# Kernel optimization log

Measured on AMD Instinct MI355X. Metric: run time of the kernel, lower is better.

## Reference

```python
import jax, jax.numpy as jnp
import numpy as np

N, E = 50000, 600000
DIN, DMID, DATTR, DOUT, DEMB, DH, K = 128, 128, 32, 128, 256, 768, 16


def setup_inputs() -> dict:
    key = jax.random.key(0)
    ks = jax.random.split(key, 12)
    s = lambda d: 1.0 / np.sqrt(d)
    return {
        "x": jax.random.normal(ks[0], (N, DIN), jnp.float32),
        "attributes": jax.random.normal(ks[1], (N, DATTR), jnp.float32),
        "edge_weight": jax.random.uniform(ks[2], (E,), jnp.float32),
        "hidden_state": jax.random.normal(ks[3], (1, DH), jnp.float32),
        "edge_index": jax.random.randint(ks[4], (2, E), 0, N, jnp.int64),
        "W1": jax.random.normal(ks[5], (DIN, DMID), jnp.float32) * s(DIN),
        "b1": jnp.zeros((DMID,), jnp.float32),
        "W2": jax.random.normal(ks[6], (DMID + DATTR, DOUT), jnp.float32) * s(DMID + DATTR),
        "b2": jnp.zeros((DOUT,), jnp.float32),
        "Wmap": jax.random.normal(ks[7], (DOUT + DATTR, DEMB), jnp.float32) * s(DOUT + DATTR),
        "bmap": jnp.zeros((DEMB,), jnp.float32),
        "Wattn": jax.random.normal(ks[8], (DH, DOUT + DATTR), jnp.float32) * s(DH),
    }


def gcn_conv(x, W, b, src, dst, w, n):
    """PyG GCNConv with normalize=True: A_hat = D^-1/2 (A+I) D^-1/2, out = A_hat X W + b."""
    loop = jnp.arange(n, dtype=src.dtype)
    src2 = jnp.concatenate([src, loop])
    dst2 = jnp.concatenate([dst, loop])
    w2 = jnp.concatenate([w, jnp.ones((n,), x.dtype)])
    deg = jax.ops.segment_sum(w2, dst2, num_segments=n)
    dinv = jnp.where(deg > 0, jax.lax.rsqrt(jnp.maximum(deg, 1e-12)), 0.0)
    norm = dinv[src2] * w2 * dinv[dst2]        # [E+N]
    h = x @ W                                   # [n, out] transform first (small dim)
    msg = h[src2] * norm[:, None]               # gather + scale, [E+N, out]
    return jax.ops.segment_sum(msg, dst2, num_segments=n) + b


def reference(x, attributes, edge_weight, hidden_state, edge_index,
              W1, b1, W2, b2, Wmap, bmap, Wattn):
    n = x.shape[0]
    src, dst = edge_index[0], edge_index[1]
    h = jax.nn.relu(gcn_conv(x, W1, b1, src, dst, edge_weight, n))
    # F.dropout with training=False is identity (module run in eval mode)
    h = jnp.concatenate([h, attributes], axis=1)           # [N, DMID+DATTR]
    h = gcn_conv(h, W2, b2, src, dst, edge_weight, n)      # [N, DOUT]
    h = jnp.concatenate([h, attributes], axis=1)           # [N, DOUT+DATTR]
    # DotAttnChoseImportentNode: project hidden state, dot with node feats, take top-K nodes
    q = hidden_state @ Wattn                                # [1, DOUT+DATTR]
    scores = h @ q[0]                                       # [N]
    _, idx = jax.lax.top_k(scores, K)
    chose_nodes = h[idx].reshape(1, -1)                     # [1, K*(DOUT+DATTR)]
    # final_mapping: mean-pool graph embed + linear
    emb = jnp.mean(h, axis=0, keepdims=True) @ Wmap + bmap  # [1, DEMB]
    return jnp.concatenate([emb, chose_nodes], axis=1)      # [1, DEMB + K*(DOUT+DATTR)]
```

## Files before the change

### kernel.cpp

```cpp
#include <hip/hip_runtime.h>

#define N_NODES 50000
#define N_EDGES 600000
#define D_IN 128
#define D_MID 128
#define D_ATTR 32
#define D_OUT 128
#define D_EMB 256
#define D_H 768
#define K_TOP 16
#define D_CAT (D_OUT + D_ATTR)
#define N_CHUNKBLKS 196
#define N_CAND (N_CHUNKBLKS * K_TOP)
#define CSLOTS 13
#define WSCALE 262144.0f
#define CS_BLOCKS 768

__global__ void k_init(unsigned long long* packed, float* q) {
    int i = blockIdx.x * blockDim.x + threadIdx.x;
    if (i < N_NODES) packed[i] = 0ULL;
    if (i < D_CAT)   q[i] = 0.0f;
}

__global__ void k_deg(const int* __restrict__ dst, const float* __restrict__ w,
                      unsigned long long* __restrict__ packed) {
    int e = blockIdx.x * blockDim.x + threadIdx.x;
    if (e < N_EDGES) {
        int d = dst[e];
        unsigned long long q = (1ULL << 40)
                             + (unsigned long long)__float2uint_rn(w[e] * WSCALE);
        atomicAdd(&packed[d], q);
    }
}

__global__ __launch_bounds__(256) void k_scan_blk(const unsigned long long* __restrict__ packed,
                                                  float* __restrict__ dinv,
                                                  int* __restrict__ incl,
                                                  int* __restrict__ bsum) {
    __shared__ int sm[256];
    int tid = threadIdx.x;
    int i = blockIdx.x * 256 + tid;
    unsigned long long p = (i < N_NODES) ? packed[i] : 0ULL;
    int v = (int)(p >> 40);
    if (i < N_NODES) {
        float wsum = (float)(p & 0xFFFFFFFFFFULL) * (1.0f / WSCALE);
        dinv[i] = rsqrtf(1.0f + wsum);
    }
    sm[tid] = v;
    __syncthreads();
    for (int off = 1; off < 256; off <<= 1) {
        int t = (tid >= off) ? sm[tid - off] : 0;
        __syncthreads();
        sm[tid] += t;
        __syncthreads();
    }
    if (i < N_NODES) incl[i] = sm[tid];
    if (tid == 255) bsum[blockIdx.x] = sm[255];
}

__global__ __launch_bounds__(256) void k_scan_top(const int* __restrict__ bsum,
                                                  int* __restrict__ boff) {
    __shared__ int sm[256];
    int tid = threadIdx.x;
    int v = (tid < N_CHUNKBLKS) ? bsum[tid] : 0;
    sm[tid] = v;
    __syncthreads();
    for (int off = 1; off < 256; off <<= 1) {
        int t = (tid >= off) ? sm[tid - off] : 0;
        __syncthreads();
        sm[tid] += t;
        __syncthreads();
    }
    if (tid < N_CHUNKBLKS) boff[tid] = sm[tid] - v;
}

__global__ __launch_bounds__(256) void k_scan_add(const int* __restrict__ incl,
                                                  const int* __restrict__ boff,
                                                  const unsigned long long* __restrict__ packed,
                                                  int* __restrict__ row_ptr,
                                                  int* __restrict__ cursor) {
    int i = blockIdx.x * 256 + threadIdx.x;
    if (i < N_NODES) {
        int ip = incl[i] + boff[blockIdx.x];
        row_ptr[i + 1] = ip;
        cursor[i] = ip - (int)(packed[i] >> 40);
        if (i == 0) row_ptr[0] = 0;
    }
}

__global__ void k_fill(const int* __restrict__ src, const int* __restrict__ dst,
                       const float* __restrict__ w, const float* __restrict__ dinv,
                       int* __restrict__ cursor, int2* __restrict__ recs) {
    int e = blockIdx.x * blockDim.x + threadIdx.x;
    if (e < N_EDGES) {
        int s = src[e], d = dst[e];
        int pos = atomicAdd(&cursor[d], 1);
        float nr = dinv[s] * w[e] * dinv[d];
        recs[pos] = make_int2(s, __float_as_int(nr));
    }
}

#define GBM 64
#define GBK 32
__global__ __launch_bounds__(256) void k_gemm(
    const float* __restrict__ in1, int d1,
    const float* __restrict__ in2, int d2,
    const float* __restrict__ W,
    float* __restrict__ out)
{
    __shared__ float xs[GBM][GBK + 1];
    __shared__ float ws[GBK][128];
    int tid = threadIdx.x;
    int cx = tid & 7;
    int ry = tid >> 3;
    int row0 = blockIdx.x * GBM;
    float acc[2][16];
#pragma unroll
    for (int i = 0; i < 2; ++i)
#pragma unroll
        for (int j = 0; j < 16; ++j) acc[i][j] = 0.0f;
    int KD = d1 + d2;
    for (int kt = 0; kt < KD; kt += GBK) {
        const float* srcp; int sd, scol;
        if (kt < d1) { srcp = in1; sd = d1; scol = kt; }
        else         { srcp = in2; sd = d2; scol = kt - d1; }
#pragma unroll
        for (int i = 0; i < 2; ++i) {
            int vid = tid + i * 256;
            int rr = vid >> 3;
            int kc = (vid & 7) * 4;
            int r = row0 + rr;
            float4 val = make_float4(0.f, 0.f, 0.f, 0.f);
            if (r < N_NODES)
                val = *(const float4*)(srcp + (size_t)r * sd + scol + kc);
            xs[rr][kc + 0] = val.x;
            xs[rr][kc + 1] = val.y;
            xs[rr][kc + 2] = val.z;
            xs[rr][kc + 3] = val.w;
        }
#pragma unroll
        for (int i = 0; i < 4; ++i) {
            int vid = tid + i * 256;
            int kk = vid >> 5;
            int c = (vid & 31) * 4;
            *(float4*)&ws[kk][c] = *(const float4*)(W + (size_t)(kt + kk) * 128 + c);
        }
        __syncthreads();
#pragma unroll
        for (int kk = 0; kk < GBK; ++kk) {
            float xv0 = xs[ry * 2 + 0][kk];
            float xv1 = xs[ry * 2 + 1][kk];
            float wv[16];
#pragma unroll
            for (int j4 = 0; j4 < 4; ++j4)
                *(float4*)&wv[j4 * 4] = *(float4*)&ws[kk][cx * 4 + j4 * 32];
#pragma unroll
            for (int j = 0; j < 16; ++j) {
                acc[0][j] += xv0 * wv[j];
                acc[1][j] += xv1 * wv[j];
            }
        }
        __syncthreads();
    }
#pragma unroll
    for (int i = 0; i < 2; ++i) {
        int r = row0 + ry * 2 + i;
        if (r < N_NODES) {
#pragma unroll
            for (int j4 = 0; j4 < 4; ++j4)
                *(float4*)(out + (size_t)r * 128 + cx * 4 + j4 * 32)
                    = *(float4*)&acc[i][j4 * 4];
        }
    }
}

__global__ __launch_bounds__(256) void k_agg(
    const float* __restrict__ t, const float* __restrict__ dinv,
    const int* __restrict__ row_ptr, const int2* __restrict__ recs,
    const float* __restrict__ bias,
    float* __restrict__ out, int relu_flag,
    const float* __restrict__ attr, const float* __restrict__ q,
    float* __restrict__ scores, int score_flag)
{
    int lane = threadIdx.x & 63;
    int node = blockIdx.x * 4 + (threadIdx.x >> 6);
    if (node >= N_NODES) return;
    const float2* t2 = (const float2*)t;
    float di = dinv[node];
    float sw = di * di;
    float2 v = t2[(size_t)node * 64 + lane];
    float accx = v.x * sw, accy = v.y * sw;
    int e0 = row_ptr[node], e1 = row_ptr[node + 1];
    int len = e1 - e0;
    for (int base = 0; base < len; base += 64) {
        int m = len - base; if (m > 64) m = 64;
        int2 myrec = make_int2(0, 0);
        if (lane < m) myrec = recs[e0 + base + lane];
        int j = 0;
        for (; j + 8 <= m; j += 8) {
            int   s0 = __shfl(myrec.x, j + 0, 64), s1 = __shfl(myrec.x, j + 1, 64);
            int   s2 = __shfl(myrec.x, j + 2, 64), s3 = __shfl(myrec.x, j + 3, 64);
            int   s4 = __shfl(myrec.x, j + 4, 64), s5 = __shfl(myrec.x, j + 5, 64);
            int   s6 = __shfl(myrec.x, j + 6, 64), s7 = __shfl(myrec.x, j + 7, 64);
            float w0 = __int_as_float(__shfl(myrec.y, j + 0, 64));
            float w1 = __int_as_float(__shfl(myrec.y, j + 1, 64));
            float w2 = __int_as_float(__shfl(myrec.y, j + 2, 64));
            float w3 = __int_as_float(__shfl(myrec.y, j + 3, 64));
            float w4 = __int_as_float(__shfl(myrec.y, j + 4, 64));
            float w5 = __int_as_float(__shfl(myrec.y, j + 5, 64));
            float w6 = __int_as_float(__shfl(myrec.y, j + 6, 64));
            float w7 = __int_as_float(__shfl(myrec.y, j + 7, 64));
            float2 u0 = t2[(size_t)s0 * 64 + lane];
            float2 u1 = t2[(size_t)s1 * 64 + lane];
            float2 u2 = t2[(size_t)s2 * 64 + lane];
            float2 u3 = t2[(size_t)s3 * 64 + lane];
            float2 u4 = t2[(size_t)s4 * 64 + lane];
            float2 u5 = t2[(size_t)s5 * 64 + lane];
            float2 u6 = t2[(size_t)s6 * 64 + lane];
            float2 u7 = t2[(size_t)s7 * 64 + lane];
            accx += w0 * u0.x + w1 * u1.x + w2 * u2.x + w3 * u3.x
                  + w4 * u4.x + w5 * u5.x + w6 * u6.x + w7 * u7.x;
            accy += w0 * u0.y + w1 * u1.y + w2 * u2.y + w3 * u3.y
                  + w4 * u4.y + w5 * u5.y + w6 * u6.y + w7 * u7.y;
        }
        for (; j + 4 <= m; j += 4) {
            int s0 = __shfl(myrec.x, j + 0, 64);
            int s1 = __shfl(myrec.x, j + 1, 64);
            int s2 = __shfl(myrec.x, j + 2, 64);
            int s3 = __shfl(myrec.x, j + 3, 64);
            float w0 = __int_as_float(__shfl(myrec.y, j + 0, 64));
            float w1 = __int_as_float(__shfl(myrec.y, j + 1, 64));
            float w2 = __int_as_float(__shfl(myrec.y, j + 2, 64));
            float w3 = __int_as_float(__shfl(myrec.y, j + 3, 64));
            float2 u0 = t2[(size_t)s0 * 64 + lane];
            float2 u1 = t2[(size_t)s1 * 64 + lane];
            float2 u2 = t2[(size_t)s2 * 64 + lane];
            float2 u3 = t2[(size_t)s3 * 64 + lane];
            accx += w0 * u0.x + w1 * u1.x + w2 * u2.x + w3 * u3.x;
            accy += w0 * u0.y + w1 * u1.y + w2 * u2.y + w3 * u3.y;
        }
        for (; j < m; ++j) {
            int s = __shfl(myrec.x, j, 64);
            float wn = __int_as_float(__shfl(myrec.y, j, 64));
            float2 u = t2[(size_t)s * 64 + lane];
            accx += wn * u.x;
            accy += wn * u.y;
        }
    }
    const float2* b2 = (const float2*)bias;
    float2 bb = b2[lane];
    accx += bb.x; accy += bb.y;
    if (relu_flag) {
        accx = fmaxf(accx, 0.0f);
        accy = fmaxf(accy, 0.0f);
    }
    float2 res; res.x = accx; res.y = accy;
    ((float2*)out)[(size_t)node * 64 + lane] = res;
    if (score_flag) {
        const float2* q2 = (const float2*)q;
        float2 qq = q2[lane];
        float s = accx * qq.x + accy * qq.y;
        if (lane < 16) {
            const float2* at2 = (const float2*)attr;
            float2 a = at2[(size_t)node * 16 + lane];
            float2 qa = q2[64 + lane];
            s += a.x * qa.x + a.y * qa.y;
        }
        for (int off = 32; off; off >>= 1) s += __shfl_xor(s, off, 64);
        if (lane == 0) scores[node] = s;
    }
}

__global__ void k_q(const float* __restrict__ hs, const float* __restrict__ Wattn,
                    float* __restrict__ q) {
    int j = threadIdx.x;
    if (j >= D_CAT) return;
    int k0 = blockIdx.x * (D_H / 8);
    float acc = 0.0f;
    for (int k = k0; k < k0 + D_H / 8; k++) acc += hs[k] * Wattn[k * D_CAT + j];
    atomicAdd(&q[j], acc);
}

__global__ __launch_bounds__(256) void k_colsum_partial(const float* __restrict__ h2,
                                                        const float* __restrict__ attr,
                                                        float* __restrict__ partial) {
    __shared__ float4 sm[256];
    int tid = threadIdx.x;
    int per = (N_NODES + CS_BLOCKS - 1) / CS_BLOCKS;
    int r0 = blockIdx.x * per;
    int r1 = min(N_NODES, r0 + per);
    float* myrow = partial + (size_t)blockIdx.x * D_CAT;
    {
        const float4* h4 = (const float4*)h2;
        int c = tid & 31;
        float4 acc = make_float4(0.f, 0.f, 0.f, 0.f);
        for (int r = r0 + (tid >> 5); r < r1; r += 8) {
            float4 v = h4[(size_t)r * 32 + c];
            acc.x += v.x; acc.y += v.y; acc.z += v.z; acc.w += v.w;
        }
        sm[tid] = acc;
        __syncthreads();
        if (tid < 32) {
            float4 s = sm[tid];
#pragma unroll
            for (int g = 1; g < 8; ++g) {
                float4 v = sm[g * 32 + tid];
                s.x += v.x; s.y += v.y; s.z += v.z; s.w += v.w;
            }
            ((float4*)myrow)[tid] = s;
        }
        __syncthreads();
    }
    {
        const float4* a4 = (const float4*)attr;
        int c = tid & 7;
        float4 acc = make_float4(0.f, 0.f, 0.f, 0.f);
        for (int r = r0 + (tid >> 3); r < r1; r += 32) {
            float4 v = a4[(size_t)r * 8 + c];
            acc.x += v.x; acc.y += v.y; acc.z += v.z; acc.w += v.w;
        }
        sm[tid] = acc;
        __syncthreads();
        if (tid < 8) {
            float4 s = sm[tid];
#pragma unroll
            for (int g = 1; g < 32; ++g) {
                float4 v = sm[g * 8 + tid];
                s.x += v.x; s.y += v.y; s.z += v.z; s.w += v.w;
            }
            ((float4*)(myrow + D_OUT))[tid] = s;
        }
    }
}

__global__ __launch_bounds__(256) void k_colsum_reduce(const float* __restrict__ partial,
                                                       float* __restrict__ colsum) {
    __shared__ float4 sm[256];
    int tid = threadIdx.x;
    int cg = blockIdx.x;
    float4 acc = make_float4(0.f, 0.f, 0.f, 0.f);
#pragma unroll
    for (int k = 0; k < 3; ++k) {
        int b = tid + k * 256;
        float4 v = *(const float4*)(partial + (size_t)b * D_CAT + cg * 4);
        acc.x += v.x; acc.y += v.y; acc.z += v.z; acc.w += v.w;
    }
    sm[tid] = acc;
    __syncthreads();
    for (int off = 128; off; off >>= 1) {
        if (tid < off) {
            float4 v = sm[tid + off];
            sm[tid].x += v.x; sm[tid].y += v.y; sm[tid].z += v.z; sm[tid].w += v.w;
        }
        __syncthreads();
    }
    if (tid == 0) *(float4*)(colsum + cg * 4) = sm[0];
}

__global__ __launch_bounds__(256) void k_top1(const float* __restrict__ scores,
                                              float* __restrict__ cand_s,
                                              int* __restrict__ cand_i) {
    int tid = threadIdx.x;
    int lane = tid & 63;
    int wave = tid >> 6;
    int i = blockIdx.x * 256 + tid;
    float s = (i < N_NODES) ? scores[i] : -INFINITY;
    int ix = i;
    __shared__ float wls[4];
    __shared__ int   wli[4];
    __shared__ int   fin_i;
    for (int it = 0; it < K_TOP; ++it) {
        float bs = s; int bi = ix;
#pragma unroll
        for (int off = 32; off; off >>= 1) {
            float s2 = __shfl_xor(bs, off, 64);
            int   i2 = __shfl_xor(bi, off, 64);
            if (s2 > bs || (s2 == bs && i2 < bi)) { bs = s2; bi = i2; }
        }
        if (lane == 0) { wls[wave] = bs; wli[wave] = bi; }
        __syncthreads();
        if (tid == 0) {
            float f = wls[0]; int fi = wli[0];
#pragma unroll
            for (int w = 1; w < 4; ++w)
                if (wls[w] > f || (wls[w] == f && wli[w] < fi)) { f = wls[w]; fi = wli[w]; }
            cand_s[blockIdx.x * K_TOP + it] = f;
            cand_i[blockIdx.x * K_TOP + it] = fi;
            fin_i = fi;
        }
        __syncthreads();
        if (ix == fin_i) s = -INFINITY;
    }
}

__global__ __launch_bounds__(256) void k_top2emb(
    const float* __restrict__ cand_s, const int* __restrict__ cand_i,
    const float* __restrict__ colsum, const float* __restrict__ Wmap,
    const float* __restrict__ bmap,
    const float* __restrict__ h2, const float* __restrict__ attr,
    float* __restrict__ out)
{
    float s[CSLOTS]; int ix[CSLOTS];
    int tid = threadIdx.x;
    int lane = tid & 63;
    int wave = tid >> 6;
#pragma unroll
    for (int j = 0; j < CSLOTS; ++j) {
        int c = tid + j * 256;
        s[j]  = (c < N_CAND) ? cand_s[c] : -INFINITY;
        ix[j] = (c < N_CAND) ? cand_i[c] : 0x7fffffff;
    }
    __shared__ float wsum_s[4];
    __shared__ int   wsum_i[4];
    __shared__ int   win_i;
    __shared__ int   ti[K_TOP];
    for (int it = 0; it < K_TOP; ++it) {
        float bs = -INFINITY; int bi = 0x7fffffff;
#pragma unroll
        for (int j = 0; j < CSLOTS; ++j) {
            if (s[j] > bs || (s[j] == bs && ix[j] < bi)) { bs = s[j]; bi = ix[j]; }
        }
#pragma unroll
        for (int off = 32; off; off >>= 1) {
            float s2 = __shfl_xor(bs, off, 64);
            int   i2 = __shfl_xor(bi, off, 64);
            if (s2 > bs || (s2 == bs && i2 < bi)) { bs = s2; bi = i2; }
        }
        if (lane == 0) { wsum_s[wave] = bs; wsum_i[wave] = bi; }
        __syncthreads();
        if (tid == 0) {
            float ws0 = wsum_s[0]; int wi0 = wsum_i[0];
#pragma unroll
            for (int w = 1; w < 4; ++w) {
                float s2 = wsum_s[w]; int i2 = wsum_i[w];
                if (s2 > ws0 || (s2 == ws0 && i2 < wi0)) { ws0 = s2; wi0 = i2; }
            }
            win_i = wi0;
            ti[it] = wi0;
        }
        __syncthreads();
        int w = win_i;
#pragma unroll
        for (int j = 0; j < CSLOTS; ++j)
            if (ix[j] == w) s[j] = -INFINITY;
        __syncthreads();
    }
    __shared__ float cs[D_CAT];
    if (tid < D_CAT) cs[tid] = colsum[tid];
    __syncthreads();
    float acc = 0.0f;
#pragma unroll 8
    for (int k = 0; k < D_CAT; ++k) acc += cs[k] * Wmap[k * D_EMB + tid];
    out[tid] = acc * (1.0f / N_NODES) + bmap[tid];
    for (int idx = tid; idx < K_TOP * D_CAT; idx += 256) {
        int kk = idx / D_CAT;
        int d = idx % D_CAT;
        int node = ti[kk];
        out[D_EMB + idx] = (d < D_OUT) ? h2[node * D_OUT + d]
                                       : attr[node * D_ATTR + (d - D_OUT)];
    }
}

extern "C" void kernel_launch(void* const* d_in, const int* in_sizes, int n_in,
                              void* d_out, int out_size, void* d_ws, size_t ws_size,
                              hipStream_t stream) {
    const float* x      = (const float*)d_in[0];
    const float* attr   = (const float*)d_in[1];
    const float* ew     = (const float*)d_in[2];
    const float* hs     = (const float*)d_in[3];
    const int*   ei     = (const int*)d_in[4];
    const float* W1     = (const float*)d_in[5];
    const float* b1     = (const float*)d_in[6];
    const float* W2     = (const float*)d_in[7];
    const float* b2     = (const float*)d_in[8];
    const float* Wmap   = (const float*)d_in[9];
    const float* bmap   = (const float*)d_in[10];
    const float* Wattn  = (const float*)d_in[11];
    float* out = (float*)d_out;
    const int* e_src = ei;
    const int* e_dst = ei + N_EDGES;

    size_t off = 0;
    auto alloc = [&](size_t bytes) {
        void* p = (char*)d_ws + off;
        off += (bytes + 255) / 256 * 256;
        return p;
    };
    unsigned long long* packed = (unsigned long long*)alloc((size_t)N_NODES * 8);
    float* dinv   = (float*)alloc((size_t)N_NODES * 4);
    int*   rowp   = (int*)  alloc((size_t)(N_NODES + 1) * 4);
    int*   cursor = (int*)  alloc((size_t)N_NODES * 4);
    int2*  recs   = (int2*) alloc((size_t)N_EDGES * 8);
    float* bufA   = (float*)alloc((size_t)N_NODES * 128 * 4);
    float* bufB   = (float*)alloc((size_t)N_NODES * 128 * 4);
    float* scores = (float*)alloc((size_t)N_NODES * 4);
    float* q      = (float*)alloc(D_CAT * 4);
    float* colsum = (float*)alloc(D_CAT * 4);
    float* partial= (float*)alloc((size_t)CS_BLOCKS * D_CAT * 4);
    float* cand_s = (float*)alloc((size_t)N_CAND * 4);
    int*   cand_i = (int*)  alloc((size_t)N_CAND * 4);
    int*   incl   = (int*)  alloc((size_t)N_NODES * 4);
    int*   bsum   = (int*)  alloc((size_t)N_CHUNKBLKS * 4);
    int*   boff   = (int*)  alloc((size_t)N_CHUNKBLKS * 4);

    int nblk = (N_NODES + 255) / 256;
    int eblk = (N_EDGES + 255) / 256;

    hipLaunchKernelGGL(k_init, dim3(nblk), dim3(256), 0, stream, packed, q);
    hipLaunchKernelGGL(k_deg, dim3(eblk), dim3(256), 0, stream, e_dst, ew, packed);
    hipLaunchKernelGGL(k_scan_blk, dim3(nblk), dim3(256), 0, stream, packed, dinv, incl, bsum);
    hipLaunchKernelGGL(k_scan_top, dim3(1), dim3(256), 0, stream, bsum, boff);
    hipLaunchKernelGGL(k_scan_add, dim3(nblk), dim3(256), 0, stream, incl, boff, packed,
                       rowp, cursor);
    hipLaunchKernelGGL(k_fill, dim3(eblk), dim3(256), 0, stream, e_src, e_dst, ew, dinv,
                       cursor, recs);
    hipLaunchKernelGGL(k_q, dim3(8), dim3(192), 0, stream, hs, Wattn, q);
    hipLaunchKernelGGL(k_gemm, dim3((N_NODES + GBM - 1) / GBM), dim3(256), 0, stream,
                       x, D_IN, x, 0, W1, bufA);
    hipLaunchKernelGGL(k_agg, dim3((N_NODES + 3) / 4), dim3(256), 0, stream,
                       bufA, dinv, rowp, recs, b1, bufB, 1,
                       (const float*)nullptr, (const float*)nullptr, (float*)nullptr, 0);
    hipLaunchKernelGGL(k_gemm, dim3((N_NODES + GBM - 1) / GBM), dim3(256), 0, stream,
                       bufB, D_MID, attr, D_ATTR, W2, bufA);
    hipLaunchKernelGGL(k_agg, dim3((N_NODES + 3) / 4), dim3(256), 0, stream,
                       bufA, dinv, rowp, recs, b2, bufB, 0,
                       attr, q, scores, 1);
    hipLaunchKernelGGL(k_colsum_partial, dim3(CS_BLOCKS), dim3(256), 0, stream,
                       bufB, attr, partial);
    hipLaunchKernelGGL(k_colsum_reduce, dim3(D_CAT / 4), dim3(256), 0, stream,
                       partial, colsum);
    hipLaunchKernelGGL(k_top1, dim3(N_CHUNKBLKS), dim3(256), 0, stream,
                       scores, cand_s, cand_i);
    hipLaunchKernelGGL(k_top2emb, dim3(1), dim3(256), 0, stream,
                       cand_s, cand_i, colsum, Wmap, bmap, bufB, attr, out);
}
```

Baseline: 302.5 us.

## Slice aggregation by column, derive CSR slots from degree atomics, move scoring into colsum

The degree kernel now records each edge's rank from the atomicAdd return value, so the CSR fill computes positions as rowp[d]+rank[e] and no longer needs a second atomic pass over cursors. The aggregation kernel is rebuilt so each block handles one 16-column slice for four nodes. Each wave splits its edges across four lane groups, and the partial sums are combined with xor shuffles, giving 8x more blocks with narrower scalar gathers. Score computation moves out of the aggregation kernel into the column-sum kernel, which already reads h2 and attributes. The trade-offs are an extra 600K-int rank array, an 8x re-read of the edge records per node, and scalar instead of float2 gathers.

```diff
diff --git a/kernel.cpp b/kernel.cpp
--- a/kernel.cpp
+++ b/kernel.cpp
@@ -23,13 +23,14 @@
 }
 
 __global__ void k_deg(const int* __restrict__ dst, const float* __restrict__ w,
-                      unsigned long long* __restrict__ packed) {
+                      unsigned long long* __restrict__ packed, int* __restrict__ rank) {
     int e = blockIdx.x * blockDim.x + threadIdx.x;
     if (e < N_EDGES) {
         int d = dst[e];
-        unsigned long long q = (1ULL << 40)
-                             + (unsigned long long)__float2uint_rn(w[e] * WSCALE);
-        atomicAdd(&packed[d], q);
+        unsigned long long qv = (1ULL << 40)
+                              + (unsigned long long)__float2uint_rn(w[e] * WSCALE);
+        unsigned long long old = atomicAdd(&packed[d], qv);
+        rank[e] = (int)(old >> 40);
     }
 }
 
@@ -76,25 +77,22 @@
 
 __global__ __launch_bounds__(256) void k_scan_add(const int* __restrict__ incl,
                                                   const int* __restrict__ boff,
-                                                  const unsigned long long* __restrict__ packed,
-                                                  int* __restrict__ row_ptr,
-                                                  int* __restrict__ cursor) {
+                                                  int* __restrict__ row_ptr) {
     int i = blockIdx.x * 256 + threadIdx.x;
     if (i < N_NODES) {
-        int ip = incl[i] + boff[blockIdx.x];
-        row_ptr[i + 1] = ip;
-        cursor[i] = ip - (int)(packed[i] >> 40);
+        row_ptr[i + 1] = incl[i] + boff[blockIdx.x];
         if (i == 0) row_ptr[0] = 0;
     }
 }
 
 __global__ void k_fill(const int* __restrict__ src, const int* __restrict__ dst,
-                       const float* __restrict__ w, const float* __restrict__ dinv,
-                       int* __restrict__ cursor, int2* __restrict__ recs) {
+                       const float* __restrict__ w, const int* __restrict__ rank,
+                       const float* __restrict__ dinv, const int* __restrict__ rowp,
+                       int2* __restrict__ recs) {
     int e = blockIdx.x * blockDim.x + threadIdx.x;
     if (e < N_EDGES) {
         int s = src[e], d = dst[e];
-        int pos = atomicAdd(&cursor[d], 1);
+        int pos = rowp[d] + rank[e];
         float nr = dinv[s] * w[e] * dinv[d];
         recs[pos] = make_int2(s, __float_as_int(nr));
     }
@@ -176,99 +174,53 @@
 
 __global__ __launch_bounds__(256) void k_agg(
     const float* __restrict__ t, const float* __restrict__ dinv,
-    const int* __restrict__ row_ptr, const int2* __restrict__ recs,
+    const int* __restrict__ rowp, const int2* __restrict__ recs,
     const float* __restrict__ bias,
-    float* __restrict__ out, int relu_flag,
-    const float* __restrict__ attr, const float* __restrict__ q,
-    float* __restrict__ scores, int score_flag)
+    float* __restrict__ out, int relu_flag)
 {
-    int lane = threadIdx.x & 63;
-    int node = blockIdx.x * 4 + (threadIdx.x >> 6);
-    if (node >= N_NODES) return;
-    const float2* t2 = (const float2*)t;
-    float di = dinv[node];
-    float sw = di * di;
-    float2 v = t2[(size_t)node * 64 + lane];
-    float accx = v.x * sw, accy = v.y * sw;
-    int e0 = row_ptr[node], e1 = row_ptr[node + 1];
+    int slice = blockIdx.x & 7;
+    int ng    = blockIdx.x >> 3;
+    int wav   = threadIdx.x >> 6;
+    int lane  = threadIdx.x & 63;
+    int node  = ng * 4 + wav;
+    int j4   = lane >> 4;
+    int col  = slice * 16 + (lane & 15);
+    float acc = 0.0f;
+    int e0 = rowp[node], e1 = rowp[node + 1];
     int len = e1 - e0;
     for (int base = 0; base < len; base += 64) {
         int m = len - base; if (m > 64) m = 64;
         int2 myrec = make_int2(0, 0);
-        if (lane < m) myrec = recs[e0 + base + lane];
-        int j = 0;
-        for (; j + 8 <= m; j += 8) {
-            int   s0 = __shfl(myrec.x, j + 0, 64), s1 = __shfl(myrec.x, j + 1, 64);
-            int   s2 = __shfl(myrec.x, j + 2, 64), s3 = __shfl(myrec.x, j + 3, 64);
-            int   s4 = __shfl(myrec.x, j + 4, 64), s5 = __shfl(myrec.x, j + 5, 64);
-            int   s6 = __shfl(myrec.x, j + 6, 64), s7 = __shfl(myrec.x, j + 7, 64);
-            float w0 = __int_as_float(__shfl(myrec.y, j + 0, 64));
-            float w1 = __int_as_float(__shfl(myrec.y, j + 1, 64));
-            float w2 = __int_as_float(__shfl(myrec.y, j + 2, 64));
-            float w3 = __int_as_float(__shfl(myrec.y, j + 3, 64));
-            float w4 = __int_as_float(__shfl(myrec.y, j + 4, 64));
-            float w5 = __int_as_float(__shfl(myrec.y, j + 5, 64));
-            float w6 = __int_as_float(__shfl(myrec.y, j + 6, 64));
-            float w7 = __int_as_float(__shfl(myrec.y, j + 7, 64));
-            float2 u0 = t2[(size_t)s0 * 64 + lane];
-            float2 u1 = t2[(size_t)s1 * 64 + lane];
-            float2 u2 = t2[(size_t)s2 * 64 + lane];
-            float2 u3 = t2[(size_t)s3 * 64 + lane];
-            float2 u4 = t2[(size_t)s4 * 64 + lane];
-            float2 u5 = t2[(size_t)s5 * 64 + lane];
-            float2 u6 = t2[(size_t)s6 * 64 + lane];
-            float2 u7 = t2[(size_t)s7 * 64 + lane];
-            accx += w0 * u0.x + w1 * u1.x + w2 * u2.x + w3 * u3.x
-                  + w4 * u4.x + w5 * u5.x + w6 * u6.x + w7 * u7.x;
-            accy += w0 * u0.y + w1 * u1.y + w2 * u2.y + w3 * u3.y
-                  + w4 * u4.y + w5 * u5.y + w6 * u6.y + w7 * u7.y;
-        }
-        for (; j + 4 <= m; j += 4) {
-            int s0 = __shfl(myrec.x, j + 0, 64);
-            int s1 = __shfl(myrec.x, j + 1, 64);
-            int s2 = __shfl(myrec.x, j + 2, 64);
-            int s3 = __shfl(myrec.x, j + 3, 64);
-            float w0 = __int_as_float(__shfl(myrec.y, j + 0, 64));
-            float w1 = __int_as_float(__shfl(myrec.y, j + 1, 64));
-            float w2 = __int_as_float(__shfl(myrec.y, j + 2, 64));
-            float w3 = __int_as_float(__shfl(myrec.y, j + 3, 64));
-            float2 u0 = t2[(size_t)s0 * 64 + lane];
-            float2 u1 = t2[(size_t)s1 * 64 + lane];
-            float2 u2 = t2[(size_t)s2 * 64 + lane];
-            float2 u3 = t2[(size_t)s3 * 64 + lane];
-            accx += w0 * u0.x + w1 * u1.x + w2 * u2.x + w3 * u3.x;
-            accy += w0 * u0.y + w1 * u1.y + w2 * u2.y + w3 * u3.y;
-        }
-        for (; j < m; ++j) {
-            int s = __shfl(myrec.x, j, 64);
-            float wn = __int_as_float(__shfl(myrec.y, j, 64));
-            float2 u = t2[(size_t)s * 64 + lane];
-            accx += wn * u.x;
-            accy += wn * u.y;
-        }
-    }
-    const float2* b2 = (const float2*)bias;
-    float2 bb = b2[lane];
-    accx += bb.x; accy += bb.y;
-    if (relu_flag) {
-        accx = fmaxf(accx, 0.0f);
-        accy = fmaxf(accy, 0.0f);
-    }
-    float2 res; res.x = accx; res.y = accy;
-    ((float2*)out)[(size_t)node * 64 + lane] = res;
-    if (score_flag) {
-        const float2* q2 = (const float2*)q;
-        float2 qq = q2[lane];
-        float s = accx * qq.x + accy * qq.y;
-        if (lane < 16) {
-            const float2* at2 = (const float2*)attr;
-            float2 a = at2[(size_t)node * 16 + lane];
-            float2 qa = q2[64 + lane];
-            s += a.x * qa.x + a.y * qa.y;
-        }
-        for (int off = 32; off; off >>= 1) s += __shfl_xor(s, off, 64);
-        if (lane == 0) scores[node] = s;
-    }
+        if (lane < m) {
+            long long rl = __builtin_nontemporal_load(
+                (const long long*)&recs[e0 + base + lane]);
+            myrec.x = (int)(rl & 0xffffffffLL);
+            myrec.y = (int)(rl >> 32);
+        }
+        for (int jb = 0; jb < m; jb += 16) {
+            int ja = jb + j4, jb1 = jb + 4 + j4, jc = jb + 8 + j4, jd = jb + 12 + j4;
+            int   s0 = __shfl(myrec.x, ja, 64);
+            int   s1 = __shfl(myrec.x, jb1, 64);
+            int   s2 = __shfl(myrec.x, jc, 64);
+            int   s3 = __shfl(myrec.x, jd, 64);
+            float w0 = __int_as_float(__shfl(myrec.y, ja, 64));
+            float w1 = __int_as_float(__shfl(myrec.y, jb1, 64));
+            float w2 = __int_as_float(__shfl(myrec.y, jc, 64));
+            float w3 = __int_as_float(__shfl(myrec.y, jd, 64));
+            float u0 = t[(size_t)s0 * 128 + col];
+            float u1 = t[(size_t)s1 * 128 + col];
+            float u2 = t[(size_t)s2 * 128 + col];
+            float u3 = t[(size_t)s3 * 128 + col];
+            acc += w0 * u0 + w1 * u1 + w2 * u2 + w3 * u3;
+        }
+    }
+    acc += __shfl_xor(acc, 16, 64);
+    acc += __shfl_xor(acc, 32, 64);
+    float di = dinv[node];
+    acc += di * di * t[(size_t)node * 128 + col];
+    acc += bias[col];
+    if (relu_flag) acc = fmaxf(acc, 0.0f);
+    if (j4 == 0) out[(size_t)node * 128 + col] = acc;
 }
 
 __global__ void k_q(const float* __restrict__ hs, const float* __restrict__ Wattn,
@@ -281,10 +233,13 @@
     atomicAdd(&q[j], acc);
 }
 
-__global__ __launch_bounds__(256) void k_colsum_partial(const float* __restrict__ h2,
-                                                        const float* __restrict__ attr,
-                                                        float* __restrict__ partial) {
+__global__ __launch_bounds__(256) void k_post(const float* __restrict__ h2,
+                                              const float* __restrict__ attr,
+                                              const float* __restrict__ q,
+                                              float* __restrict__ partial,
+                                              float* __restrict__ scores) {
     __shared__ float4 sm[256];
+    __shared__ float rowsc[80];
     int tid = threadIdx.x;
     int per = (N_NODES + CS_BLOCKS - 1) / CS_BLOCKS;
     int r0 = blockIdx.x * per;
@@ -293,10 +248,15 @@
     {
         const float4* h4 = (const float4*)h2;
         int c = tid & 31;
+        float4 qv = ((const float4*)q)[c];
         float4 acc = make_float4(0.f, 0.f, 0.f, 0.f);
         for (int r = r0 + (tid >> 5); r < r1; r += 8) {
             float4 v = h4[(size_t)r * 32 + c];
             acc.x += v.x; acc.y += v.y; acc.z += v.z; acc.w += v.w;
+            float sd = v.x * qv.x + v.y * qv.y + v.z * qv.z + v.w * qv.w;
+#pragma unroll
+            for (int off = 16; off; off >>= 1) sd += __shfl_xor(sd, off, 32);
+            if (c == 0) rowsc[r - r0] = sd;
         }
         sm[tid] = acc;
         __syncthreads();
@@ -314,10 +274,15 @@
     {
         const float4* a4 = (const float4*)attr;
         int c = tid & 7;
+        float4 qv = ((const float4*)q)[32 + c];
         float4 acc = make_float4(0.f, 0.f, 0.f, 0.f);
         for (int r = r0 + (tid >> 3); r < r1; r += 32) {
             float4 v = a4[(size_t)r * 8 + c];
             acc.x += v.x; acc.y += v.y; acc.z += v.z; acc.w += v.w;
+            float sd = v.x * qv.x + v.y * qv.y + v.z * qv.z + v.w * qv.w;
+#pragma unroll
+            for (int off = 4; off; off >>= 1) sd += __shfl_xor(sd, off, 8);
+            if (c == 0) scores[r] = rowsc[r - r0] + sd;
         }
         sm[tid] = acc;
         __syncthreads();
@@ -489,7 +454,7 @@
     unsigned long long* packed = (unsigned long long*)alloc((size_t)N_NODES * 8);
     float* dinv   = (float*)alloc((size_t)N_NODES * 4);
     int*   rowp   = (int*)  alloc((size_t)(N_NODES + 1) * 4);
-    int*   cursor = (int*)  alloc((size_t)N_NODES * 4);
+    int*   rank   = (int*)  alloc((size_t)N_EDGES * 4);
     int2*  recs   = (int2*) alloc((size_t)N_EDGES * 8);
     float* bufA   = (float*)alloc((size_t)N_NODES * 128 * 4);
     float* bufB   = (float*)alloc((size_t)N_NODES * 128 * 4);
@@ -505,28 +470,26 @@
 
     int nblk = (N_NODES + 255) / 256;
     int eblk = (N_EDGES + 255) / 256;
+    int aggblk = (N_NODES / 4) * 8;
 
     hipLaunchKernelGGL(k_init, dim3(nblk), dim3(256), 0, stream, packed, q);
-    hipLaunchKernelGGL(k_deg, dim3(eblk), dim3(256), 0, stream, e_dst, ew, packed);
+    hipLaunchKernelGGL(k_deg, dim3(eblk), dim3(256), 0, stream, e_dst, ew, packed, rank);
     hipLaunchKernelGGL(k_scan_blk, dim3(nblk), dim3(256), 0, stream, packed, dinv, incl, bsum);
     hipLaunchKernelGGL(k_scan_top, dim3(1), dim3(256), 0, stream, bsum, boff);
-    hipLaunchKernelGGL(k_scan_add, dim3(nblk), dim3(256), 0, stream, incl, boff, packed,
-                       rowp, cursor);
-    hipLaunchKernelGGL(k_fill, dim3(eblk), dim3(256), 0, stream, e_src, e_dst, ew, dinv,
-                       cursor, recs);
+    hipLaunchKernelGGL(k_scan_add, dim3(nblk), dim3(256), 0, stream, incl, boff, rowp);
+    hipLaunchKernelGGL(k_fill, dim3(eblk), dim3(256), 0, stream, e_src, e_dst, ew, rank,
+                       dinv, rowp, recs);
     hipLaunchKernelGGL(k_q, dim3(8), dim3(192), 0, stream, hs, Wattn, q);
     hipLaunchKernelGGL(k_gemm, dim3((N_NODES + GBM - 1) / GBM), dim3(256), 0, stream,
                        x, D_IN, x, 0, W1, bufA);
-    hipLaunchKernelGGL(k_agg, dim3((N_NODES + 3) / 4), dim3(256), 0, stream,
-                       bufA, dinv, rowp, recs, b1, bufB, 1,
-                       (const float*)nullptr, (const float*)nullptr, (float*)nullptr, 0);
+    hipLaunchKernelGGL(k_agg, dim3(aggblk), dim3(256), 0, stream,
+                       bufA, dinv, rowp, recs, b1, bufB, 1);
     hipLaunchKernelGGL(k_gemm, dim3((N_NODES + GBM - 1) / GBM), dim3(256), 0, stream,
                        bufB, D_MID, attr, D_ATTR, W2, bufA);
-    hipLaunchKernelGGL(k_agg, dim3((N_NODES + 3) / 4), dim3(256), 0, stream,
-                       bufA, dinv, rowp, recs, b2, bufB, 0,
-                       attr, q, scores, 1);
-    hipLaunchKernelGGL(k_colsum_partial, dim3(CS_BLOCKS), dim3(256), 0, stream,
-                       bufB, attr, partial);
+    hipLaunchKernelGGL(k_agg, dim3(aggblk), dim3(256), 0, stream,
+                       bufA, dinv, rowp, recs, b2, bufB, 0);
+    hipLaunchKernelGGL(k_post, dim3(CS_BLOCKS), dim3(256), 0, stream,
+                       bufB, attr, q, partial, scores);
     hipLaunchKernelGGL(k_colsum_reduce, dim3(D_CAT / 4), dim3(256), 0, stream,
                        partial, colsum);
     hipLaunchKernelGGL(k_top1, dim3(N_CHUNKBLKS), dim3(256), 0, stream,
```

Result: slower. 435.4 us (+43.9%).
